# Optimization experiments

Measured on AMD Instinct MI355X. Metric: run time of the kernel, lower is better.

The kernel has to match this reference:

```python
import jax, jax.numpy as jnp
import numpy as np

EPS = 1e-6
NUM_HEADS = 16  # config.num_attention_heads

def _rms(h, w):
    h32 = h.astype(jnp.float32)
    v = jnp.mean(h32 * h32, axis=-1, keepdims=True)
    return (w * h32 * jax.lax.rsqrt(v + EPS)).astype(h.dtype)

def _rope(q, k, pos):
    dh = q.shape[-1]
    inv = 1.0 / (10000.0 ** (jnp.arange(0, dh, 2, dtype=jnp.float32) / dh))
    ang = pos.astype(jnp.float32)[:, None] * inv[None, :]  # [n, dh/2]
    cos = jnp.concatenate([jnp.cos(ang), jnp.cos(ang)], -1)[None, None]  # [1,1,n,dh]
    sin = jnp.concatenate([jnp.sin(ang), jnp.sin(ang)], -1)[None, None]
    def rot(x):
        x1, x2 = x[..., :dh // 2], x[..., dh // 2:]
        return jnp.concatenate([-x2, x1], -1)
    return q * cos + rot(q) * sin, k * cos + rot(k) * sin

def _skip_causal_mask(N, block_size, len1, text_len):
    qi = jnp.arange(N)[:, None]
    ki = jnp.arange(N)[None, :]
    qb = (qi - text_len) // block_size
    kb = (ki - text_len) // block_size
    iq = qi >= text_len
    ik = ki >= text_len
    return (((ki < text_len) & (qi >= ki))
            | (iq & ik & (qb < len1) & (kb < len1) & (qb >= kb))
            | (iq & ik & (qb >= len1) & (kb < len1) & (qb - len1 > kb))
            | (iq & ik & (qb == kb)))

def _layer(x, position_ids, text_position_ids, qkv_w, qkv_b, proj_w, proj_b,
           qn_w, kn_w, ln1_w, ln2_w, gate_w, up_w, down_w,
           block_size, text_len, len1):
    B, N, C = x.shape
    H = NUM_HEADS
    Dh = C // H
    T = text_len
    Lc = len1 * block_size
    offs = [0, T, T + Lc]
    lens = [T, Lc, N - T - Lc]  # text / clean / noised segment lengths
    qs, ks, vs = [], [], []
    for i in range(3):
        seg = _rms(x[:, offs[i]:offs[i] + lens[i]], ln1_w[i])  # input layernorm
        qkv = seg @ qkv_w[i] + qkv_b[i]                        # [B,n,3C]
        qkv = qkv.reshape(B, lens[i], 3, H, Dh).transpose(2, 0, 3, 1, 4)
        qs.append(_rms(qkv[0], qn_w[i]))
        ks.append(_rms(qkv[1], kn_w[i]))
        vs.append(qkv[2])
    img_q = jnp.concatenate([qs[1], qs[2]], axis=2)
    img_k = jnp.concatenate([ks[1], ks[2]], axis=2)
    img_q, img_k = _rope(img_q, img_k, position_ids)
    txt_q, txt_k = _rope(qs[0], ks[0], text_position_ids)
    q = jnp.concatenate([txt_q, img_q], axis=2)
    k = jnp.concatenate([txt_k, img_k], axis=2)
    v = jnp.concatenate(vs, axis=2)
    scores = jnp.einsum('bhqd,bhkd->bhqk', q, k) / np.float32(np.sqrt(Dh))
    mask = _skip_causal_mask(N, block_size, len1, text_len)
    scores = jnp.where(mask, scores, jnp.finfo(scores.dtype).min)
    attn = jax.nn.softmax(scores, axis=-1)
    o = jnp.einsum('bhqk,bhkd->bhqd', attn, v)
    o = o.transpose(0, 2, 1, 3).reshape(B, N, C)
    o = jnp.concatenate([o[:, offs[i]:offs[i] + lens[i]] @ proj_w[i] + proj_b[i]
                         for i in range(3)], axis=1)
    h = x + o
    mlp = []
    for i in range(3):
        y = _rms(h[:, offs[i]:offs[i] + lens[i]], ln2_w[i])  # post-attn layernorm
        mlp.append((jax.nn.silu(y @ gate_w[i]) * (y @ up_w[i])) @ down_w[i])
    return h + jnp.concatenate(mlp, axis=1)

def setup_inputs():
    key = jax.random.key(0)
    ks = jax.random.split(key, 8)
    B, C, H, I = 2, 1024, 16, 4096
    block_size, text_len, len1, len2 = 128, 256, 4, 4
    N = text_len + (len1 + len2) * block_size  # 1280
    s = 0.02
    return {
        'x': jax.random.normal(ks[0], (B, N, C), jnp.float32),
        'position_ids': jnp.arange((len1 + len2) * block_size, dtype=jnp.int32),
        'text_position_ids': jnp.arange(text_len, dtype=jnp.int32),
        'qkv_w': jax.random.normal(ks[1], (3, C, 3 * C), jnp.float32) * s,
        'qkv_b': jnp.zeros((3, 3 * C), jnp.float32),
        'proj_w': jax.random.normal(ks[2], (3, C, C), jnp.float32) * s,
        'proj_b': jnp.zeros((3, C), jnp.float32),
        'qn_w': jnp.ones((3, C // H), jnp.float32),
        'kn_w': jnp.ones((3, C // H), jnp.float32),
        'ln1_w': jnp.ones((3, C), jnp.float32),
        'ln2_w': jnp.ones((3, C), jnp.float32),
        'gate_w': jax.random.normal(ks[3], (3, C, I), jnp.float32) * s,
        'up_w': jax.random.normal(ks[4], (3, C, I), jnp.float32) * s,
        'down_w': jax.random.normal(ks[5], (3, I, C), jnp.float32) * s,
        'block_size': block_size, 'text_len': text_len, 'len1': len1,
    }

def reference(x, position_ids, text_position_ids, qkv_w, qkv_b, proj_w, proj_b,
              qn_w, kn_w, ln1_w, ln2_w, gate_w, up_w, down_w,
              block_size, text_len, len1):
    return _layer(x, position_ids, text_position_ids, qkv_w, qkv_b, proj_w, proj_b,
                  qn_w, kn_w, ln1_w, ln2_w, gate_w, up_w, down_w,
                  block_size, text_len, len1)
```

## Files before the change

### kernel.cpp

```cpp
#include <hip/hip_runtime.h>
#include <math.h>

constexpr int Bb  = 2;
constexpr int Nn  = 1280;
constexpr int Cc  = 1024;
constexpr int Hh  = 16;
constexpr int DH  = 64;
constexpr int Ii  = 4096;
constexpr int Tt  = 256;
constexpr int BSz = 128;
constexpr int L1  = 4;
constexpr int Mrows = Bb * Nn;

typedef __attribute__((ext_vector_type(8))) short short8v;
typedef __attribute__((ext_vector_type(4))) float f32x4;

__device__ __forceinline__ int segof(int n) {
    return n < Tt ? 0 : (n < Tt + L1 * BSz ? 1 : 2);
}
__device__ __forceinline__ unsigned short f2bf(float f) {
    unsigned int u = __float_as_uint(f);
    u += 0x7fffu + ((u >> 16) & 1u);
    return (unsigned short)(u >> 16);
}
__device__ __forceinline__ float bf2f(unsigned short h) {
    return __uint_as_float(((unsigned int)h) << 16);
}

__device__ __forceinline__ int xcd_swz(int lin, int nwg) {
    int cpx = nwg >> 3;
    return (lin & 7) * cpx + (lin >> 3);
}

__device__ __forceinline__ void rms_dev(const float* __restrict__ in,
                                        const float* __restrict__ w,
                                        unsigned short* __restrict__ out,
                                        int row, float* sred) {
    int n   = row % Nn;
    int seg = segof(n);
    const float* x = in + (size_t)row * Cc;
    int t = threadIdx.x;
    float4 xv = reinterpret_cast<const float4*>(x)[t];
    float ss = xv.x * xv.x + xv.y * xv.y + xv.z * xv.z + xv.w * xv.w;
#pragma unroll
    for (int off = 32; off; off >>= 1) ss += __shfl_down(ss, off, 64);
    int lane = t & 63, wid = t >> 6;
    if (lane == 0) sred[wid] = ss;
    __syncthreads();
    if (t == 0) sred[4] = rsqrtf((sred[0] + sred[1] + sred[2] + sred[3]) * (1.0f / Cc) + 1e-6f);
    __syncthreads();
    float r = sred[4];
    float4 wv = reinterpret_cast<const float4*>(w + (size_t)seg * Cc)[t];
    ushort4 ov;
    ov.x = f2bf(wv.x * xv.x * r);
    ov.y = f2bf(wv.y * xv.y * r);
    ov.z = f2bf(wv.z * xv.z * r);
    ov.w = f2bf(wv.w * xv.w * r);
    *reinterpret_cast<ushort4*>(&out[(size_t)row * Cc + t * 4]) = ov;
}

__device__ __forceinline__ void pack_dev(const float* __restrict__ W,
                                         unsigned short* __restrict__ PB,
                                         int K, int Nd, size_t idx) {
    size_t cpseg = (size_t)K * Nd / 8;
    int s = (int)(idx / cpseg);
    size_t rm = idx % cpseg;
    int lane = (int)(rm & 63);
    int fr   = (int)((rm >> 6) & 7);
    size_t tile = rm >> 9;
    int nct = Nd >> 7;
    int cb = (int)(tile % nct);
    int kt = (int)(tile / nct);
    int col = cb * 128 + fr * 16 + (lane & 15);
    int k0  = kt * 32 + (lane >> 4) * 8;
    const float* src = W + ((size_t)s * K + k0) * Nd + col;
    unsigned short o[8];
#pragma unroll
    for (int j = 0; j < 8; j++) o[j] = f2bf(src[(size_t)j * Nd]);
    short8v v;
#pragma unroll
    for (int j = 0; j < 8; j++) v[j] = (short)o[j];
    *reinterpret_cast<short8v*>(&PB[idx * 8]) = v;
}

__global__ __launch_bounds__(256)
void pack_w(const float* __restrict__ W, unsigned short* __restrict__ PB,
            int K, int Nd) {
    pack_dev(W, PB, K, Nd, (size_t)blockIdx.x * 256 + threadIdx.x);
}

__global__ __launch_bounds__(256)
void fat1(const float* __restrict__ x, const float* __restrict__ ln1_w,
          unsigned short* __restrict__ xn,
          const float* __restrict__ qkv_w, unsigned short* __restrict__ qkv_p) {
    __shared__ float sred[5];
    int bid = blockIdx.x;
    if (bid < Mrows) {
        rms_dev(x, ln1_w, xn, bid, sred);
    } else {
        pack_dev(qkv_w, qkv_p, Cc, 3 * Cc, (size_t)(bid - Mrows) * 256 + threadIdx.x);
    }
}

__device__ __forceinline__ void attn_dev(
        const unsigned short* __restrict__ Qg, const unsigned short* __restrict__ Kg,
        const unsigned short* __restrict__ Vg, unsigned short* __restrict__ O,
        int qt, int bh,
        unsigned short* k_lds, unsigned short* vt_lds, unsigned short* p_base) {
    int b = bh >> 4, h = bh & 15;
    int tid = threadIdx.x, lane = tid & 63, wid = tid >> 6;
    int g = lane >> 4, c = lane & 15;

    const size_t headoff = (size_t)bh * Nn * DH;
    int q0 = qt * 64;
    bool qtext = q0 < Tt;
    int qb = qtext ? 0 : (q0 - Tt) / BSz;

    int qrow_frag = q0 + wid * 16 + c;
    short8v aq[2];
#pragma unroll
    for (int kb = 0; kb < 2; kb++)
        aq[kb] = *reinterpret_cast<const short8v*>(
            &Qg[headoff + (size_t)qrow_frag * DH + kb * 32 + g * 8]);

    unsigned short* pbuf = p_base + wid * 1024;

    f32x4 o_[4];
#pragma unroll
    for (int nb = 0; nb < 4; nb++) o_[nb] = (f32x4){0.f, 0.f, 0.f, 0.f};
    float m_[4] = {-3.4e38f, -3.4e38f, -3.4e38f, -3.4e38f};
    float l_[4] = {0.f, 0.f, 0.f, 0.f};

    int tr = tid >> 2, tc = tid & 3;

    for (int kt = 0; kt < Nn / 64; kt++) {
        int kbase = kt * 64;
        bool vis, diag = false;
        if (qtext) {
            vis = (kbase <= q0);
            diag = (kbase == q0);
        } else if (kbase < Tt) {
            vis = true;
        } else {
            int kb = (kbase - Tt) / BSz;
            vis = (qb < L1) ? (kb <= qb)
                            : ((kb < L1 && qb - L1 > kb) || kb == qb);
        }
        if (!vis) continue;

        __syncthreads();
        {
            const unsigned short* ks = &Kg[headoff + (size_t)(kbase + tr) * DH];
            const unsigned short* vs = &Vg[headoff + (size_t)(kbase + tr) * DH];
#pragma unroll
            for (int i = 0; i < 2; i++) {
                int ch = tc + i * 4;
                short8v kv = *reinterpret_cast<const short8v*>(ks + ch * 8);
                int byte = (tr * 128 + ch * 16) ^ ((tr & 7) << 4);
                *reinterpret_cast<short8v*>((char*)k_lds + byte) = kv;
                short8v vv = *reinterpret_cast<const short8v*>(vs + ch * 8);
#pragma unroll
                for (int j = 0; j < 8; j++) {
                    int dh = ch * 8 + j;
                    int vbyte = (dh * 128 + tr * 2) ^ ((dh & 7) << 4);
                    *reinterpret_cast<unsigned short*>((char*)vt_lds + vbyte) =
                        (unsigned short)vv[j];
                }
            }
        }
        __syncthreads();

        f32x4 s_[4];
#pragma unroll
        for (int nb = 0; nb < 4; nb++) s_[nb] = (f32x4){0.f, 0.f, 0.f, 0.f};
#pragma unroll
        for (int nb = 0; nb < 4; nb++) {
            int kil = nb * 16 + c;
#pragma unroll
            for (int kb = 0; kb < 2; kb++) {
                int byte = (kil * 128 + kb * 64 + g * 16) ^ ((kil & 7) << 4);
                short8v bk = *reinterpret_cast<short8v*>((char*)k_lds + byte);
                s_[nb] = __builtin_amdgcn_mfma_f32_16x16x32_bf16(aq[kb], bk, s_[nb], 0, 0, 0);
            }
        }
#pragma unroll
        for (int nb = 0; nb < 4; nb++) {
#pragma unroll
            for (int r = 0; r < 4; r++) {
                float sv = s_[nb][r] * 0.125f;
                if (diag) {
                    int qrl = wid * 16 + g * 4 + r;
                    int kcl = nb * 16 + c;
                    if (qrl < kcl) sv = -3.4e38f;
                }
                s_[nb][r] = sv;
            }
        }
#pragma unroll
        for (int r = 0; r < 4; r++) {
            float mx = fmaxf(fmaxf(s_[0][r], s_[1][r]), fmaxf(s_[2][r], s_[3][r]));
#pragma unroll
            for (int off = 1; off <= 8; off <<= 1)
                mx = fmaxf(mx, __shfl_xor(mx, off, 64));
            float mn = fmaxf(m_[r], mx);
            float es = __expf(m_[r] - mn);
            m_[r] = mn;
            float pv[4];
            float rs = 0.f;
#pragma unroll
            for (int nb = 0; nb < 4; nb++) {
                pv[nb] = __expf(s_[nb][r] - mn);
                rs += pv[nb];
            }
#pragma unroll
            for (int off = 1; off <= 8; off <<= 1)
                rs += __shfl_xor(rs, off, 64);
            l_[r] = l_[r] * es + rs;
#pragma unroll
            for (int nb = 0; nb < 4; nb++) o_[nb][r] *= es;
            int qrl = g * 4 + r;
            int swz = (qrl & 7) << 4;
#pragma unroll
            for (int nb = 0; nb < 4; nb++) {
                int byte = (qrl * 128 + (nb * 16 + c) * 2) ^ swz;
                *reinterpret_cast<unsigned short*>((char*)pbuf + byte) = f2bf(pv[nb]);
            }
        }
        short8v aP[2];
#pragma unroll
        for (int kb = 0; kb < 2; kb++) {
            int byte = (c * 128 + kb * 64 + g * 16) ^ ((c & 7) << 4);
            aP[kb] = *reinterpret_cast<short8v*>((char*)pbuf + byte);
        }
#pragma unroll
        for (int nb = 0; nb < 4; nb++) {
            int dh = nb * 16 + c;
#pragma unroll
            for (int kb = 0; kb < 2; kb++) {
                int byte = (dh * 128 + kb * 64 + g * 16) ^ ((dh & 7) << 4);
                short8v bv = *reinterpret_cast<short8v*>((char*)vt_lds + byte);
                o_[nb] = __builtin_amdgcn_mfma_f32_16x16x32_bf16(aP[kb], bv, o_[nb], 0, 0, 0);
            }
        }
    }

    float inv_[4];
#pragma unroll
    for (int r = 0; r < 4; r++) inv_[r] = 1.f / l_[r];
#pragma unroll
    for (int nb = 0; nb < 4; nb++) {
        int col = h * DH + nb * 16 + c;
#pragma unroll
        for (int r = 0; r < 4; r++) {
            int row = q0 + wid * 16 + g * 4 + r;
            O[((size_t)b * Nn + row) * Cc + col] = f2bf(o_[nb][r] * inv_[r]);
        }
    }
}

__global__ __launch_bounds__(256)
void fat2(const unsigned short* __restrict__ Qg, const unsigned short* __restrict__ Kg,
          const unsigned short* __restrict__ Vg, unsigned short* __restrict__ O,
          const float* __restrict__ proj_w, unsigned short* __restrict__ proj_p,
          const float* __restrict__ gate_w, unsigned short* __restrict__ gate_p,
          const float* __restrict__ up_w,   unsigned short* __restrict__ up_p) {
    __shared__ __align__(16) unsigned short k_lds[64 * 64];
    __shared__ __align__(16) unsigned short vt_lds[64 * 64];
    __shared__ __align__(16) unsigned short p_lds[4 * 16 * 64];
    int bid = blockIdx.x;
    if (bid < 640) {
        attn_dev(Qg, Kg, Vg, O, bid % 20, bid / 20, k_lds, vt_lds, p_lds);
        return;
    }
    bid -= 640;
    if (bid < 1536) {
        pack_dev(proj_w, proj_p, Cc, Cc, (size_t)bid * 256 + threadIdx.x);
        return;
    }
    bid -= 1536;
    if (bid < 6144) {
        pack_dev(gate_w, gate_p, Cc, Ii, (size_t)bid * 256 + threadIdx.x);
        return;
    }
    bid -= 6144;
    pack_dev(up_w, up_p, Cc, Ii, (size_t)bid * 256 + threadIdx.x);
}

template <int OUTMODE, bool BIAS, int NZ>
__global__ __launch_bounds__(256, 2)
void gemm128r(const unsigned short* __restrict__ A,
              const unsigned short* __restrict__ PB,
              const float* __restrict__ bias, void* __restrict__ outp,
              int K, int Nd) {
    __shared__ __align__(16) unsigned short lds[8192];
    int bx = blockIdx.x, by = blockIdx.y, bz = (NZ > 1) ? blockIdx.z : 0;
    {
        int gx = gridDim.x, gy = gridDim.y, gz = (NZ > 1) ? gridDim.z : 1;
        int lin = bx + gx * (by + gy * bz);
        int swz = xcd_swz(lin, gx * gy * gz);
        bx = swz % gx; swz /= gx;
        by = swz % gy; bz = swz / gy;
    }
    int rb = bx * 128, cb = by;
    int seg = segof(rb % Nn);
    int tid = threadIdx.x, lane = tid & 63, wid = tid >> 6;
    int wr = wid >> 1, wc = wid & 1;
    int g = lane >> 4, c_ = lane & 15;
    const int nct = Nd >> 7;
    const int Keff = K / NZ;
    const int nKt = Keff >> 5;
    const int kz = bz * Keff;
    const unsigned short* PBseg = PB + (size_t)seg * K * Nd;

    int mf0 = tid >> 6, lc0 = tid & 63;
    const unsigned short* pA0 =
        A + (size_t)(rb + mf0 * 16 + (lc0 & 15)) * K + kz + (lc0 >> 4) * 8;
    const unsigned short* pA1 = pA0 + (size_t)64 * K;
    const unsigned short* pB0 =
        PBseg + (((size_t)(kz >> 5) * nct + cb) * 8 + mf0) * 512 + (size_t)lc0 * 8;
    const unsigned short* pB1 = pB0 + 2048;
    const size_t bstep = (size_t)nct * 4096;

    f32x4 acc[4][4];
#pragma unroll
    for (int m = 0; m < 4; m++)
#pragma unroll
        for (int n = 0; n < 4; n++) acc[m][n] = (f32x4){0.f, 0.f, 0.f, 0.f};

    short8v av[2], bv[2];
    av[0] = *reinterpret_cast<const short8v*>(pA0);
    av[1] = *reinterpret_cast<const short8v*>(pA1);
    bv[0] = *reinterpret_cast<const short8v*>(pB0);
    bv[1] = *reinterpret_cast<const short8v*>(pB1);
    pA0 += 32; pA1 += 32; pB0 += bstep; pB1 += bstep;

    for (int kt = 0; kt < nKt; ++kt) {
        __syncthreads();
        *reinterpret_cast<short8v*>(&lds[(size_t)tid * 8]) = av[0];
        *reinterpret_cast<short8v*>(&lds[(size_t)(tid + 256) * 8]) = av[1];
        *reinterpret_cast<short8v*>(&lds[4096 + (size_t)tid * 8]) = bv[0];
        *reinterpret_cast<short8v*>(&lds[4096 + (size_t)(tid + 256) * 8]) = bv[1];
        __syncthreads();
        if (kt + 1 < nKt) {
            av[0] = *reinterpret_cast<const short8v*>(pA0);
            av[1] = *reinterpret_cast<const short8v*>(pA1);
            bv[0] = *reinterpret_cast<const short8v*>(pB0);
            bv[1] = *reinterpret_cast<const short8v*>(pB1);
            pA0 += 32; pA1 += 32; pB0 += bstep; pB1 += bstep;
        }
        short8v afr[4], bfr[4];
#pragma unroll
        for (int m = 0; m < 4; m++)
            afr[m] = *reinterpret_cast<short8v*>(&lds[((wr * 4 + m) * 64 + lane) * 8]);
#pragma unroll
        for (int n = 0; n < 4; n++)
            bfr[n] = *reinterpret_cast<short8v*>(&lds[4096 + ((wc * 4 + n) * 64 + lane) * 8]);
#pragma unroll
        for (int m = 0; m < 4; m++)
#pragma unroll
            for (int n = 0; n < 4; n++)
                acc[m][n] = __builtin_amdgcn_mfma_f32_16x16x32_bf16(
                    afr[m], bfr[n], acc[m][n], 0, 0, 0);
    }

    float* outf = (float*)outp;
    unsigned short* outh = (unsigned short*)outp;
    size_t zoff = (NZ > 1) ? (size_t)bz * Mrows * Nd : 0;
#pragma unroll
    for (int n = 0; n < 4; n++) {
        int col = cb * 128 + wc * 64 + n * 16 + c_;
        float bvv = BIAS ? bias[(size_t)seg * Nd + col] : 0.f;
#pragma unroll
        for (int m = 0; m < 4; m++) {
#pragma unroll
            for (int r = 0; r < 4; r++) {
                int row = rb + wr * 64 + m * 16 + g * 4 + r;
                float v = acc[m][n][r] + bvv;
                if (OUTMODE == 0) outf[zoff + (size_t)row * Nd + col] = v;
                else              outh[zoff + (size_t)row * Nd + col] = f2bf(v);
            }
        }
    }
}

__global__ __launch_bounds__(256)
void gemm_gu(const unsigned short* __restrict__ A,
             const unsigned short* __restrict__ PG,
             const unsigned short* __restrict__ PU,
             unsigned short* __restrict__ outp) {
    __shared__ __align__(16) unsigned short lds[10240];
    int bx = blockIdx.x, by = blockIdx.y;
    {
        int lin = bx + gridDim.x * by;
        int swz = xcd_swz(lin, gridDim.x * gridDim.y);
        bx = swz % gridDim.x; by = swz / gridDim.x;
    }
    int rb = bx * 64, cb = by;
    int seg = segof(rb % Nn);
    int tid = threadIdx.x, lane = tid & 63, wid = tid >> 6;
    int g = lane >> 4, c_ = lane & 15;
    const int nct = Ii >> 7;
    const unsigned short* PGseg = PG + (size_t)seg * Cc * Ii;
    const unsigned short* PUseg = PU + (size_t)seg * Cc * Ii;

    f32x4 accG[4][2], accU[4][2];
#pragma unroll
    for (int m = 0; m < 4; m++)
#pragma unroll
        for (int n = 0; n < 2; n++) {
            accG[m][n] = (f32x4){0.f, 0.f, 0.f, 0.f};
            accU[m][n] = (f32x4){0.f, 0.f, 0.f, 0.f};
        }

    int mf0 = tid >> 6, lc0 = tid & 63;
    const unsigned short* gA =
        &A[(size_t)(rb + mf0 * 16 + (lc0 & 15)) * Cc + (lc0 >> 4) * 8];
    short8v av, gv[2], uv[2];
    auto load_tile = [&](int kt) {
        av = *reinterpret_cast<const short8v*>(gA + kt * 32);
#pragma unroll
        for (int i = 0; i < 2; i++) {
            int c = tid + i * 256;
            int cf = c >> 6, lc = c & 63;
            size_t off = (((size_t)kt * nct + cb) * 8 + cf) * 64 * 8 + (size_t)lc * 8;
            gv[i] = *reinterpret_cast<const short8v*>(PGseg + off);
            uv[i] = *reinterpret_cast<const short8v*>(PUseg + off);
        }
    };

    const int nKt = Cc >> 5;
    load_tile(0);
    for (int kt = 0; kt < nKt; ++kt) {
        __syncthreads();
        *reinterpret_cast<short8v*>(&lds[(size_t)tid * 8]) = av;
#pragma unroll
        for (int i = 0; i < 2; i++) {
            *reinterpret_cast<short8v*>(&lds[2048 + (size_t)(tid + i * 256) * 8]) = gv[i];
            *reinterpret_cast<short8v*>(&lds[6144 + (size_t)(tid + i * 256) * 8]) = uv[i];
        }
        __syncthreads();
        if (kt + 1 < nKt) load_tile(kt + 1);
        short8v afr[4], gfr[2], ufr[2];
#pragma unroll
        for (int m = 0; m < 4; m++)
            afr[m] = *reinterpret_cast<short8v*>(&lds[((m) * 64 + lane) * 8]);
#pragma unroll
        for (int n = 0; n < 2; n++) {
            gfr[n] = *reinterpret_cast<short8v*>(&lds[2048 + ((wid * 2 + n) * 64 + lane) * 8]);
            ufr[n] = *reinterpret_cast<short8v*>(&lds[6144 + ((wid * 2 + n) * 64 + lane) * 8]);
        }
#pragma unroll
        for (int m = 0; m < 4; m++)
#pragma unroll
            for (int n = 0; n < 2; n++) {
                accG[m][n] = __builtin_amdgcn_mfma_f32_16x16x32_bf16(
                    afr[m], gfr[n], accG[m][n], 0, 0, 0);
                accU[m][n] = __builtin_amdgcn_mfma_f32_16x16x32_bf16(
                    afr[m], ufr[n], accU[m][n], 0, 0, 0);
            }
    }

#pragma unroll
    for (int n = 0; n < 2; n++) {
        int col = cb * 128 + (wid * 2 + n) * 16 + c_;
#pragma unroll
        for (int m = 0; m < 4; m++) {
#pragma unroll
            for (int r = 0; r < 4; r++) {
                int row = rb + m * 16 + g * 4 + r;
                float gval = accG[m][n][r], uval = accU[m][n][r];
                float t = gval / (1.f + __expf(-gval)) * uval;
                outp[(size_t)row * Ii + col] = f2bf(t);
            }
        }
    }
}

__global__ __launch_bounds__(256)
void combine_rms(const float* __restrict__ x, const float* __restrict__ bias,
                 const float* __restrict__ p, const float* __restrict__ ln2_w,
                 float* __restrict__ out, unsigned short* __restrict__ y) {
    int row = blockIdx.x;
    int n   = row % Nn;
    int seg = segof(n);
    int t   = threadIdx.x;
    size_t i = (size_t)row * 256 + t;
    float4 a  = reinterpret_cast<const float4*>(x)[i];
    float4 b  = *reinterpret_cast<const float4*>(&bias[(size_t)seg * Cc + t * 4]);
    float4 p0 = reinterpret_cast<const float4*>(p)[i];
    float4 p1 = reinterpret_cast<const float4*>(p)[i + Mrows * Cc / 4];
    float4 h;
    h.x = a.x + b.x + p0.x + p1.x;
    h.y = a.y + b.y + p0.y + p1.y;
    h.z = a.z + b.z + p0.z + p1.z;
    h.w = a.w + b.w + p0.w + p1.w;
    reinterpret_cast<float4*>(out)[i] = h;
    float ss = h.x * h.x + h.y * h.y + h.z * h.z + h.w * h.w;
#pragma unroll
    for (int off = 32; off; off >>= 1) ss += __shfl_down(ss, off, 64);
    __shared__ float sred[5];
    int lane = t & 63, wid = t >> 6;
    if (lane == 0) sred[wid] = ss;
    __syncthreads();
    if (t == 0) sred[4] = rsqrtf((sred[0] + sred[1] + sred[2] + sred[3]) * (1.0f / Cc) + 1e-6f);
    __syncthreads();
    float r = sred[4];
    float4 wv = reinterpret_cast<const float4*>(ln2_w + (size_t)seg * Cc)[t];
    ushort4 ov;
    ov.x = f2bf(wv.x * h.x * r);
    ov.y = f2bf(wv.y * h.y * r);
    ov.z = f2bf(wv.z * h.z * r);
    ov.w = f2bf(wv.w * h.w * r);
    *reinterpret_cast<ushort4*>(&y[(size_t)row * Cc + t * 4]) = ov;
}

__global__ __launch_bounds__(256)
void combine_down4(const unsigned short* __restrict__ p,
                   float* __restrict__ out) {
    int i = blockIdx.x * 256 + threadIdx.x;
    float4 a = reinterpret_cast<const float4*>(out)[i];
#pragma unroll
    for (int z = 0; z < 4; z++) {
        ushort4 u = *reinterpret_cast<const ushort4*>(&p[(size_t)z * Mrows * Cc + i * 4]);
        a.x += bf2f(u.x); a.y += bf2f(u.y); a.z += bf2f(u.z); a.w += bf2f(u.w);
    }
    reinterpret_cast<float4*>(out)[i] = a;
}

__global__ __launch_bounds__(256)
void split_rope(const unsigned short* __restrict__ qkv,
                const float* __restrict__ qn_w, const float* __restrict__ kn_w,
                const int* __restrict__ pos_ids, const int* __restrict__ tpos_ids,
                unsigned short* __restrict__ Q, unsigned short* __restrict__ K,
                unsigned short* __restrict__ V) {
    int row = blockIdx.x;
    int b = row / Nn, n = row % Nn;
    int seg = segof(n);
    int lane = threadIdx.x & 63, wid = threadIdx.x >> 6;
    int pos = (n < Tt) ? tpos_ids[n] : pos_ids[n - Tt];
    int j = lane & 31;
    float ang = (float)pos * exp2f(-(float)j * (13.287712379549449f / 32.f));
    float cv = cosf(ang), sv = sinf(ang);
    float qw = qn_w[seg * DH + lane], kw = kn_w[seg * DH + lane];
    for (int h = wid; h < Hh; h += 4) {
        const unsigned short* base = qkv + (size_t)row * (3 * Cc) + h * DH + lane;
        float q = bf2f(base[0]), k = bf2f(base[Cc]), v = bf2f(base[2 * Cc]);
        float qs = q * q, ks = k * k;
#pragma unroll
        for (int off = 32; off; off >>= 1) {
            qs += __shfl_xor(qs, off, 64);
            ks += __shfl_xor(ks, off, 64);
        }
        q = q * rsqrtf(qs * (1.f / DH) + 1e-6f) * qw;
        k = k * rsqrtf(ks * (1.f / DH) + 1e-6f) * kw;
        float qp = __shfl_xor(q, 32, 64);
        float kp = __shfl_xor(k, 32, 64);
        float qo = q * cv + ((lane < 32) ? -qp * sv : qp * sv);
        float ko = k * cv + ((lane < 32) ? -kp * sv : kp * sv);
        size_t oidx = ((size_t)(b * Hh + h) * Nn + n) * DH + lane;
        Q[oidx] = f2bf(qo);
        K[oidx] = f2bf(ko);
        V[oidx] = f2bf(v);
    }
}

extern "C" void kernel_launch(void* const* d_in, const int* in_sizes, int n_in,
                              void* d_out, int out_size, void* d_ws, size_t ws_size,
                              hipStream_t stream) {
    const float* x        = (const float*)d_in[0];
    const int*   pos_ids  = (const int*)d_in[1];
    const int*   tpos_ids = (const int*)d_in[2];
    const float* qkv_w    = (const float*)d_in[3];
    const float* qkv_b    = (const float*)d_in[4];
    const float* proj_w   = (const float*)d_in[5];
    const float* proj_b   = (const float*)d_in[6];
    const float* qn_w     = (const float*)d_in[7];
    const float* kn_w     = (const float*)d_in[8];
    const float* ln1_w    = (const float*)d_in[9];
    const float* ln2_w    = (const float*)d_in[10];
    const float* gate_w   = (const float*)d_in[11];
    const float* up_w     = (const float*)d_in[12];
    const float* down_w   = (const float*)d_in[13];
    float* out = (float*)d_out;
    char*  wsb = (char*)d_ws;

    unsigned short* WA  = (unsigned short*)(wsb);
    unsigned short* WB  = (unsigned short*)(wsb + 25165824);
    unsigned short* Tb  = (unsigned short*)(wsb + 50331648);
    unsigned short* P3  = (unsigned short*)(wsb + 71303168);
    unsigned short* P4  = (unsigned short*)(wsb + 76546048);
    unsigned short* Qbf = Tb;
    unsigned short* Kbf = Tb + 2621440;
    unsigned short* Vbf = Tb + 5242880;

    fat1<<<Mrows + 4608, 256, 0, stream>>>(x, ln1_w, P3, qkv_w, WA);
    gemm128r<1, true, 1><<<dim3(Mrows / 128, 24), 256, 0, stream>>>(
        P3, WA, qkv_b, WB, Cc, 3 * Cc);
    split_rope<<<Mrows, 256, 0, stream>>>(WB, qn_w, kn_w, pos_ids, tpos_ids,
                                          Qbf, Kbf, Vbf);
    fat2<<<640 + 1536 + 6144 + 6144, 256, 0, stream>>>(
        Qbf, Kbf, Vbf, P3, proj_w, P4, gate_w, WA, up_w, WB);
    gemm128r<0, false, 2><<<dim3(Mrows / 128, 8, 2), 256, 0, stream>>>(
        P3, P4, nullptr, (float*)Tb, Cc, Cc);
    combine_rms<<<Mrows, 256, 0, stream>>>(x, proj_b, (float*)Tb, ln2_w, out, P3);
    gemm_gu<<<dim3(Mrows / 64, 32), 256, 0, stream>>>(P3, WA, WB, Tb);
    pack_w<<<6144, 256, 0, stream>>>(down_w, WA, Ii, Cc);
    gemm128r<1, false, 4><<<dim3(Mrows / 128, 8, 4), 256, 0, stream>>>(
        Tb, WA, nullptr, WB, Ii, Cc);
    combine_down4<<<Mrows * Cc / 1024, 256, 0, stream>>>(WB, out);
}
```

Measured before the change: 247.2 us.

## Add MFMA priority hints, double-buffer GEMM prefetch, retile gate/up, split-K proj in bf16

The attention kernel raises wave priority around its MFMA blocks so matrix work is issued ahead of other waves. The generic GEMM now keeps two register prefetch stages and walks the K loop two tiles per iteration, which assumes an even tile count. The gate/up GEMM changes its wave layout from 1x4 to 2x2 so each wave loads fewer A fragments relative to B. The projection GEMM becomes a 4-way split-K writing bf16 partials, and combine_rms sums four bf16 partials instead of two fp32 ones. That last change cuts partial-sum traffic and adds parallelism but gives up some precision.

Measured after the change: 242.1 us. -2.1%, faster.

```diff
diff --git a/kernel.cpp b/kernel.cpp
--- a/kernel.cpp
+++ b/kernel.cpp
@@ -173,6 +173,7 @@
         f32x4 s_[4];
 #pragma unroll
         for (int nb = 0; nb < 4; nb++) s_[nb] = (f32x4){0.f, 0.f, 0.f, 0.f};
+        __builtin_amdgcn_s_setprio(1);
 #pragma unroll
         for (int nb = 0; nb < 4; nb++) {
             int kil = nb * 16 + c;
@@ -183,6 +184,7 @@
                 s_[nb] = __builtin_amdgcn_mfma_f32_16x16x32_bf16(aq[kb], bk, s_[nb], 0, 0, 0);
             }
         }
+        __builtin_amdgcn_s_setprio(0);
 #pragma unroll
         for (int nb = 0; nb < 4; nb++) {
 #pragma unroll
@@ -232,6 +234,7 @@
             int byte = (c * 128 + kb * 64 + g * 16) ^ ((c & 7) << 4);
             aP[kb] = *reinterpret_cast<short8v*>((char*)pbuf + byte);
         }
+        __builtin_amdgcn_s_setprio(1);
 #pragma unroll
         for (int nb = 0; nb < 4; nb++) {
             int dh = nb * 16 + c;
@@ -242,6 +245,7 @@
                 o_[nb] = __builtin_amdgcn_mfma_f32_16x16x32_bf16(aP[kb], bv, o_[nb], 0, 0, 0);
             }
         }
+        __builtin_amdgcn_s_setprio(0);
     }
 
     float inv_[4];
@@ -327,27 +331,20 @@
 #pragma unroll
         for (int n = 0; n < 4; n++) acc[m][n] = (f32x4){0.f, 0.f, 0.f, 0.f};
 
-    short8v av[2], bv[2];
-    av[0] = *reinterpret_cast<const short8v*>(pA0);
-    av[1] = *reinterpret_cast<const short8v*>(pA1);
-    bv[0] = *reinterpret_cast<const short8v*>(pB0);
-    bv[1] = *reinterpret_cast<const short8v*>(pB1);
+    short8v avA0, avA1, bvA0, bvA1;
+    short8v avB0, avB1, bvB0, bvB1;
+    avA0 = *reinterpret_cast<const short8v*>(pA0);
+    avA1 = *reinterpret_cast<const short8v*>(pA1);
+    bvA0 = *reinterpret_cast<const short8v*>(pB0);
+    bvA1 = *reinterpret_cast<const short8v*>(pB1);
     pA0 += 32; pA1 += 32; pB0 += bstep; pB1 += bstep;
-
-    for (int kt = 0; kt < nKt; ++kt) {
-        __syncthreads();
-        *reinterpret_cast<short8v*>(&lds[(size_t)tid * 8]) = av[0];
-        *reinterpret_cast<short8v*>(&lds[(size_t)(tid + 256) * 8]) = av[1];
-        *reinterpret_cast<short8v*>(&lds[4096 + (size_t)tid * 8]) = bv[0];
-        *reinterpret_cast<short8v*>(&lds[4096 + (size_t)(tid + 256) * 8]) = bv[1];
-        __syncthreads();
-        if (kt + 1 < nKt) {
-            av[0] = *reinterpret_cast<const short8v*>(pA0);
-            av[1] = *reinterpret_cast<const short8v*>(pA1);
-            bv[0] = *reinterpret_cast<const short8v*>(pB0);
-            bv[1] = *reinterpret_cast<const short8v*>(pB1);
-            pA0 += 32; pA1 += 32; pB0 += bstep; pB1 += bstep;
-        }
+    avB0 = *reinterpret_cast<const short8v*>(pA0);
+    avB1 = *reinterpret_cast<const short8v*>(pA1);
+    bvB0 = *reinterpret_cast<const short8v*>(pB0);
+    bvB1 = *reinterpret_cast<const short8v*>(pB1);
+    pA0 += 32; pA1 += 32; pB0 += bstep; pB1 += bstep;
+
+    auto compute = [&]() {
         short8v afr[4], bfr[4];
 #pragma unroll
         for (int m = 0; m < 4; m++)
@@ -361,6 +358,37 @@
             for (int n = 0; n < 4; n++)
                 acc[m][n] = __builtin_amdgcn_mfma_f32_16x16x32_bf16(
                     afr[m], bfr[n], acc[m][n], 0, 0, 0);
+    };
+
+    for (int kt = 0; kt < nKt; kt += 2) {
+        __syncthreads();
+        *reinterpret_cast<short8v*>(&lds[(size_t)tid * 8]) = avA0;
+        *reinterpret_cast<short8v*>(&lds[(size_t)(tid + 256) * 8]) = avA1;
+        *reinterpret_cast<short8v*>(&lds[4096 + (size_t)tid * 8]) = bvA0;
+        *reinterpret_cast<short8v*>(&lds[4096 + (size_t)(tid + 256) * 8]) = bvA1;
+        __syncthreads();
+        if (kt + 2 < nKt) {
+            avA0 = *reinterpret_cast<const short8v*>(pA0);
+            avA1 = *reinterpret_cast<const short8v*>(pA1);
+            bvA0 = *reinterpret_cast<const short8v*>(pB0);
+            bvA1 = *reinterpret_cast<const short8v*>(pB1);
+            pA0 += 32; pA1 += 32; pB0 += bstep; pB1 += bstep;
+        }
+        compute();
+        __syncthreads();
+        *reinterpret_cast<short8v*>(&lds[(size_t)tid * 8]) = avB0;
+        *reinterpret_cast<short8v*>(&lds[(size_t)(tid + 256) * 8]) = avB1;
+        *reinterpret_cast<short8v*>(&lds[4096 + (size_t)tid * 8]) = bvB0;
+        *reinterpret_cast<short8v*>(&lds[4096 + (size_t)(tid + 256) * 8]) = bvB1;
+        __syncthreads();
+        if (kt + 3 < nKt) {
+            avB0 = *reinterpret_cast<const short8v*>(pA0);
+            avB1 = *reinterpret_cast<const short8v*>(pA1);
+            bvB0 = *reinterpret_cast<const short8v*>(pB0);
+            bvB1 = *reinterpret_cast<const short8v*>(pB1);
+            pA0 += 32; pA1 += 32; pB0 += bstep; pB1 += bstep;
+        }
+        compute();
     }
 
     float* outf = (float*)outp;
@@ -398,16 +426,17 @@
     int rb = bx * 64, cb = by;
     int seg = segof(rb % Nn);
     int tid = threadIdx.x, lane = tid & 63, wid = tid >> 6;
+    int wr = wid >> 1, wc = wid & 1;
     int g = lane >> 4, c_ = lane & 15;
     const int nct = Ii >> 7;
     const unsigned short* PGseg = PG + (size_t)seg * Cc * Ii;
     const unsigned short* PUseg = PU + (size_t)seg * Cc * Ii;
 
-    f32x4 accG[4][2], accU[4][2];
-#pragma unroll
-    for (int m = 0; m < 4; m++)
-#pragma unroll
-        for (int n = 0; n < 2; n++) {
+    f32x4 accG[2][4], accU[2][4];
+#pragma unroll
+    for (int m = 0; m < 2; m++)
+#pragma unroll
+        for (int n = 0; n < 4; n++) {
             accG[m][n] = (f32x4){0.f, 0.f, 0.f, 0.f};
             accU[m][n] = (f32x4){0.f, 0.f, 0.f, 0.f};
         }
@@ -440,19 +469,19 @@
         }
         __syncthreads();
         if (kt + 1 < nKt) load_tile(kt + 1);
-        short8v afr[4], gfr[2], ufr[2];
-#pragma unroll
-        for (int m = 0; m < 4; m++)
-            afr[m] = *reinterpret_cast<short8v*>(&lds[((m) * 64 + lane) * 8]);
-#pragma unroll
-        for (int n = 0; n < 2; n++) {
-            gfr[n] = *reinterpret_cast<short8v*>(&lds[2048 + ((wid * 2 + n) * 64 + lane) * 8]);
-            ufr[n] = *reinterpret_cast<short8v*>(&lds[6144 + ((wid * 2 + n) * 64 + lane) * 8]);
-        }
-#pragma unroll
-        for (int m = 0; m < 4; m++)
-#pragma unroll
-            for (int n = 0; n < 2; n++) {
+        short8v afr[2], gfr[4], ufr[4];
+#pragma unroll
+        for (int m = 0; m < 2; m++)
+            afr[m] = *reinterpret_cast<short8v*>(&lds[((wr * 2 + m) * 64 + lane) * 8]);
+#pragma unroll
+        for (int n = 0; n < 4; n++) {
+            gfr[n] = *reinterpret_cast<short8v*>(&lds[2048 + ((wc * 4 + n) * 64 + lane) * 8]);
+            ufr[n] = *reinterpret_cast<short8v*>(&lds[6144 + ((wc * 4 + n) * 64 + lane) * 8]);
+        }
+#pragma unroll
+        for (int m = 0; m < 2; m++)
+#pragma unroll
+            for (int n = 0; n < 4; n++) {
                 accG[m][n] = __builtin_amdgcn_mfma_f32_16x16x32_bf16(
                     afr[m], gfr[n], accG[m][n], 0, 0, 0);
                 accU[m][n] = __builtin_amdgcn_mfma_f32_16x16x32_bf16(
@@ -461,13 +490,13 @@
     }
 
 #pragma unroll
-    for (int n = 0; n < 2; n++) {
-        int col = cb * 128 + (wid * 2 + n) * 16 + c_;
-#pragma unroll
-        for (int m = 0; m < 4; m++) {
+    for (int n = 0; n < 4; n++) {
+        int col = cb * 128 + wc * 64 + n * 16 + c_;
+#pragma unroll
+        for (int m = 0; m < 2; m++) {
 #pragma unroll
             for (int r = 0; r < 4; r++) {
-                int row = rb + m * 16 + g * 4 + r;
+                int row = rb + wr * 32 + m * 16 + g * 4 + r;
                 float gval = accG[m][n][r], uval = accU[m][n][r];
                 float t = gval / (1.f + __expf(-gval)) * uval;
                 outp[(size_t)row * Ii + col] = f2bf(t);
@@ -478,7 +507,7 @@
 
 __global__ __launch_bounds__(256)
 void combine_rms(const float* __restrict__ x, const float* __restrict__ bias,
-                 const float* __restrict__ p, const float* __restrict__ ln2_w,
+                 const unsigned short* __restrict__ p, const float* __restrict__ ln2_w,
                  float* __restrict__ out, unsigned short* __restrict__ y) {
     int row = blockIdx.x;
     int n   = row % Nn;
@@ -487,13 +516,13 @@
     size_t i = (size_t)row * 256 + t;
     float4 a  = reinterpret_cast<const float4*>(x)[i];
     float4 b  = *reinterpret_cast<const float4*>(&bias[(size_t)seg * Cc + t * 4]);
-    float4 p0 = reinterpret_cast<const float4*>(p)[i];
-    float4 p1 = reinterpret_cast<const float4*>(p)[i + Mrows * Cc / 4];
     float4 h;
-    h.x = a.x + b.x + p0.x + p1.x;
-    h.y = a.y + b.y + p0.y + p1.y;
-    h.z = a.z + b.z + p0.z + p1.z;
-    h.w = a.w + b.w + p0.w + p1.w;
+    h.x = a.x + b.x; h.y = a.y + b.y; h.z = a.z + b.z; h.w = a.w + b.w;
+#pragma unroll
+    for (int z = 0; z < 4; z++) {
+        ushort4 u = *reinterpret_cast<const ushort4*>(&p[(size_t)z * Mrows * Cc + i * 4]);
+        h.x += bf2f(u.x); h.y += bf2f(u.y); h.z += bf2f(u.z); h.w += bf2f(u.w);
+    }
     reinterpret_cast<float4*>(out)[i] = h;
     float ss = h.x * h.x + h.y * h.y + h.z * h.z + h.w * h.w;
 #pragma unroll
@@ -600,9 +629,9 @@
                                           Qbf, Kbf, Vbf);
     fat2<<<640 + 1536 + 6144 + 6144, 256, 0, stream>>>(
         Qbf, Kbf, Vbf, P3, proj_w, P4, gate_w, WA, up_w, WB);
-    gemm128r<0, false, 2><<<dim3(Mrows / 128, 8, 2), 256, 0, stream>>>(
-        P3, P4, nullptr, (float*)Tb, Cc, Cc);
-    combine_rms<<<Mrows, 256, 0, stream>>>(x, proj_b, (float*)Tb, ln2_w, out, P3);
+    gemm128r<1, false, 4><<<dim3(Mrows / 128, 8, 4), 256, 0, stream>>>(
+        P3, P4, nullptr, Tb, Cc, Cc);
+    combine_rms<<<Mrows, 256, 0, stream>>>(x, proj_b, Tb, ln2_w, out, P3);
     gemm_gu<<<dim3(Mrows / 64, 32), 256, 0, stream>>>(P3, WA, WB, Tb);
     pack_w<<<6144, 256, 0, stream>>>(down_w, WA, Ii, Cc);
     gemm128r<1, false, 4><<<dim3(Mrows / 128, 8, 4), 256, 0, stream>>>(
```
